# Performance work log

Hardware: AMD Instinct MI355X
Metric: run time of the kernel (lower is better)

The kernel has to match this reference:

```python
import jax, jax.numpy as jnp
import numpy as np

VOCAB = 100000
EMB = 128
EPS = 1e-12  # torch F.normalize eps

def setup_inputs() -> dict:
    key = jax.random.key(0)
    k1, k2, k3 = jax.random.split(key, 3)
    x = jax.random.randint(k1, (4096, 200), 0, VOCAB)
    W = jax.random.normal(k2, (EMB, VOCAB), dtype=jnp.float32) * 0.02
    b = jax.random.normal(k3, (EMB,), dtype=jnp.float32) * 0.02
    return {"x": x, "W": W, "b": b}

def reference(x, W, b):
    # one_hot(x) @ W.T + b  ==  W.T[x] + b  (row gather instead of dense matmul)
    table = W.T                      # [VOCAB, EMB]
    e = table[x] + b                 # [B, T, EMB]
    # L2 normalize along last dim (torch F.normalize p=2, eps=1e-12)
    n = jnp.sqrt(jnp.sum(e * e, axis=-1, keepdims=True))
    return e / jnp.maximum(n, EPS)
```

## Files before the change

### kernel.cpp

```cpp
#include <hip/hip_runtime.h>
#include <stdint.h>

#define EMB 128

typedef unsigned short ushort_t;
typedef ushort_t us8 __attribute__((ext_vector_type(8)));
typedef float f4 __attribute__((ext_vector_type(4)));

static __device__ __forceinline__ float bf2f(ushort_t h) {
    union { unsigned int u; float f; } cvt;
    cvt.u = ((unsigned int)h) << 16;
    return cvt.f;
}

static __device__ __forceinline__ ushort_t f2bf(float f) {
    union { float f; unsigned int u; } cvt;
    cvt.f = f;
    unsigned int u = cvt.u;
    unsigned int r = u + 0x7fffu + ((u >> 16) & 1u);
    return (ushort_t)(r >> 16);
}

__global__ __launch_bounds__(256) void build_table_f32_kernel(
    const float* __restrict__ W, const float* __restrict__ b,
    float* __restrict__ N, int vocab)
{
    __shared__ float tile[EMB][33];
    __shared__ float part[8][32];
    __shared__ float scale_s[32];

    const int v0 = blockIdx.x * 32;
    const int tx = threadIdx.x;
    const int ty = threadIdx.y;

    const int v  = v0 + tx;
    const bool vok = (v < vocab);

    #pragma unroll
    for (int e = ty; e < EMB; e += 8) {
        float w = vok ? W[(size_t)e * vocab + v] : 0.0f;
        tile[e][tx] = w + b[e];
    }
    __syncthreads();

    float ss = 0.0f;
    #pragma unroll
    for (int j = 0; j < 16; ++j) {
        float t = tile[ty * 16 + j][tx];
        ss += t * t;
    }
    part[ty][tx] = ss;
    __syncthreads();

    if (ty == 0) {
        float s = 0.0f;
        #pragma unroll
        for (int j = 0; j < 8; ++j) s += part[j][tx];
        scale_s[tx] = 1.0f / fmaxf(sqrtf(s), 1e-12f);
    }
    __syncthreads();

    const int tid = ty * 32 + tx;
    #pragma unroll
    for (int c = 0; c < 4; ++c) {
        const int chunk = tid + c * 256;
        const int r = chunk >> 5;
        const int q = chunk & 31;
        const int vv = v0 + r;
        if (vv < vocab) {
            const float sc = scale_s[r];
            f4 o;
            #pragma unroll
            for (int j = 0; j < 4; ++j) o[j] = tile[q * 4 + j][r] * sc;
            *(f4*)(N + (size_t)vv * EMB + q * 4) = o;
        }
    }
}

static __device__ __forceinline__ int detect_i64(const int* __restrict__ x32) {
    __shared__ int is64_s;
    if (threadIdx.x < 64) {
        int w = x32[2 * threadIdx.x + 1];
        unsigned long long nz = __ballot(w != 0);
        if (threadIdx.x == 0) is64_s = (nz == 0ULL) ? 1 : 0;
    }
    __syncthreads();
    return is64_s;
}

__global__ __launch_bounds__(256) void gather_copy_f32_kernel(
    const int* __restrict__ x, const float* __restrict__ N,
    float* __restrict__ out, int n_tokens, int vocab)
{
    const int is64 = detect_i64(x);
    const int tid   = blockIdx.x * blockDim.x + threadIdx.x;
    const int token = tid >> 4;
    const int l     = tid & 15;
    if (token >= n_tokens) return;

    int v = is64 ? x[2 * token] : x[token];
    v = min(max(v, 0), vocab - 1);

    const float* src = N + (size_t)v * EMB + l * 8;
    f4 a = *(const f4*)src;
    f4 c = *(const f4*)(src + 4);

    float* dst = out + (size_t)token * EMB + l * 8;
    __builtin_nontemporal_store(a, (f4*)dst);
    __builtin_nontemporal_store(c, (f4*)(dst + 4));
}

__global__ __launch_bounds__(256) void transpose_bf16_kernel(
    const float* __restrict__ W, ushort_t* __restrict__ Wt, int vocab)
{
    __shared__ float tile[32][33];
    const int v0 = blockIdx.x * 32;
    const int e0 = blockIdx.y * 32;
    const int tx = threadIdx.x;
    const int ty = threadIdx.y;

    #pragma unroll
    for (int i = 0; i < 32; i += 8) {
        int e = e0 + ty + i;
        int v = v0 + tx;
        if (e < EMB && v < vocab)
            tile[ty + i][tx] = W[(size_t)e * vocab + v];
    }
    __syncthreads();
    #pragma unroll
    for (int i = 0; i < 32; i += 8) {
        int v = v0 + ty + i;
        int e = e0 + tx;
        if (v < vocab && e < EMB)
            Wt[(size_t)v * EMB + e] = f2bf(tile[tx][ty + i]);
    }
}

static __device__ __forceinline__ void reduce_norm_store(
    float e[8], float* __restrict__ out, int token, int l)
{
    float ss = 0.0f;
    #pragma unroll
    for (int j = 0; j < 8; ++j) ss += e[j] * e[j];
    #pragma unroll
    for (int m = 1; m < 16; m <<= 1)
        ss += __shfl_xor(ss, m, 16);
    const float n = sqrtf(ss);
    const float scale = 1.0f / fmaxf(n, 1e-12f);

    f4 o0, o1;
    #pragma unroll
    for (int j = 0; j < 4; ++j) { o0[j] = e[j] * scale; o1[j] = e[j + 4] * scale; }
    float* dst = out + (size_t)token * EMB + l * 8;
    *(f4*)dst = o0;
    *(f4*)(dst + 4) = o1;
}

__global__ __launch_bounds__(256) void gather_norm_bf16_kernel(
    const int* __restrict__ x, const ushort_t* __restrict__ Wt,
    const float* __restrict__ b, float* __restrict__ out,
    int n_tokens, int vocab)
{
    const int is64 = detect_i64(x);
    const int tid   = blockIdx.x * blockDim.x + threadIdx.x;
    const int token = tid >> 4;
    const int l     = tid & 15;
    if (token >= n_tokens) return;

    int v = is64 ? x[2 * token] : x[token];
    v = min(max(v, 0), vocab - 1);

    us8 w  = *(const us8*)(Wt + (size_t)v * EMB + l * 8);
    f4 b0  = *(const f4*)(b + l * 8);
    f4 b1  = *(const f4*)(b + l * 8 + 4);

    float e[8];
    #pragma unroll
    for (int j = 0; j < 4; ++j) {
        e[j]     = bf2f(w[j])     + b0[j];
        e[j + 4] = bf2f(w[j + 4]) + b1[j];
    }
    reduce_norm_store(e, out, token, l);
}

__global__ __launch_bounds__(256) void gather_norm_direct_kernel(
    const int* __restrict__ x, const float* __restrict__ W,
    const float* __restrict__ b, float* __restrict__ out,
    int n_tokens, int vocab)
{
    const int is64 = detect_i64(x);
    const int tid   = blockIdx.x * blockDim.x + threadIdx.x;
    const int token = tid >> 4;
    const int l     = tid & 15;
    if (token >= n_tokens) return;

    int v = is64 ? x[2 * token] : x[token];
    v = min(max(v, 0), vocab - 1);

    f4 b0 = *(const f4*)(b + l * 8);
    f4 b1 = *(const f4*)(b + l * 8 + 4);

    float e[8];
    #pragma unroll
    for (int j = 0; j < 8; ++j) {
        float w = W[(size_t)(l * 8 + j) * vocab + v];
        float bj = (j < 4) ? b0[j & 3] : b1[j & 3];
        e[j] = w + bj;
    }
    reduce_norm_store(e, out, token, l);
}

extern "C" void kernel_launch(void* const* d_in, const int* in_sizes, int n_in,
                              void* d_out, int out_size, void* d_ws, size_t ws_size,
                              hipStream_t stream) {
    const int*   x = (const int*)d_in[0];
    const float* W = (const float*)d_in[1];
    const float* b = (const float*)d_in[2];
    float*     out = (float*)d_out;

    const int n_tokens = in_sizes[0];
    const int vocab    = in_sizes[1] / EMB;

    const size_t wt_f32_bytes  = (size_t)vocab * EMB * sizeof(float);
    const size_t wt_bf16_bytes = (size_t)vocab * EMB * sizeof(ushort_t);
    const int blocks = (n_tokens * 16 + 255) / 256;

    if (ws_size >= wt_f32_bytes) {
        float* N = (float*)d_ws;
        build_table_f32_kernel<<<dim3((vocab + 31) / 32), dim3(32, 8), 0, stream>>>(
            W, b, N, vocab);
        gather_copy_f32_kernel<<<blocks, 256, 0, stream>>>(x, N, out, n_tokens, vocab);
    } else if (ws_size >= wt_bf16_bytes) {
        ushort_t* Wt = (ushort_t*)d_ws;
        dim3 tb(32, 8);
        dim3 tg((vocab + 31) / 32, (EMB + 31) / 32);
        transpose_bf16_kernel<<<tg, tb, 0, stream>>>(W, Wt, vocab);
        gather_norm_bf16_kernel<<<blocks, 256, 0, stream>>>(x, Wt, b, out, n_tokens, vocab);
    } else {
        gather_norm_direct_kernel<<<blocks, 256, 0, stream>>>(x, W, b, out, n_tokens, vocab);
    }
}
```

Measured before the change: 540.2 us.

## Store normalized embedding table in fp16 and gather two tokens per thread

The precomputed bias-added, L2-normalized table is now stored in fp16 instead of fp32. This halves the table write traffic in the build kernel and the gather read traffic. The gather kernel also handles two tokens per thread (t0 and t0+half_n) to raise memory-level parallelism. The bf16 transpose fallback is removed, and the output is rounded to fp16 precision, which risks exceeding tolerance.

```diff
diff --git a/kernel.cpp b/kernel.cpp
--- a/kernel.cpp
+++ b/kernel.cpp
@@ -4,26 +4,13 @@
 #define EMB 128
 
 typedef unsigned short ushort_t;
-typedef ushort_t us8 __attribute__((ext_vector_type(8)));
+typedef _Float16 half_t;
+typedef half_t h8 __attribute__((ext_vector_type(8)));
 typedef float f4 __attribute__((ext_vector_type(4)));
 
-static __device__ __forceinline__ float bf2f(ushort_t h) {
-    union { unsigned int u; float f; } cvt;
-    cvt.u = ((unsigned int)h) << 16;
-    return cvt.f;
-}
-
-static __device__ __forceinline__ ushort_t f2bf(float f) {
-    union { float f; unsigned int u; } cvt;
-    cvt.f = f;
-    unsigned int u = cvt.u;
-    unsigned int r = u + 0x7fffu + ((u >> 16) & 1u);
-    return (ushort_t)(r >> 16);
-}
-
-__global__ __launch_bounds__(256) void build_table_f32_kernel(
+__global__ __launch_bounds__(256) void build_table_f16_kernel(
     const float* __restrict__ W, const float* __restrict__ b,
-    float* __restrict__ N, int vocab)
+    half_t* __restrict__ T, int vocab)
 {
     __shared__ float tile[EMB][33];
     __shared__ float part[8][32];
@@ -62,17 +49,18 @@
 
     const int tid = ty * 32 + tx;
     #pragma unroll
-    for (int c = 0; c < 4; ++c) {
+    for (int c = 0; c < 2; ++c) {
         const int chunk = tid + c * 256;
-        const int r = chunk >> 5;
-        const int q = chunk & 31;
+        const int r = chunk >> 4;
+        const int q = chunk & 15;
         const int vv = v0 + r;
         if (vv < vocab) {
             const float sc = scale_s[r];
-            f4 o;
+            h8 o;
             #pragma unroll
-            for (int j = 0; j < 4; ++j) o[j] = tile[q * 4 + j][r] * sc;
-            *(f4*)(N + (size_t)vv * EMB + q * 4) = o;
+            for (int j = 0; j < 8; ++j)
+                o[j] = (half_t)(tile[q * 8 + j][r] * sc);
+            *(h8*)(T + (size_t)vv * EMB + q * 8) = o;
         }
     }
 }
@@ -88,51 +76,43 @@
     return is64_s;
 }
 
-__global__ __launch_bounds__(256) void gather_copy_f32_kernel(
-    const int* __restrict__ x, const float* __restrict__ N,
+__global__ __launch_bounds__(256) void gather_copy_f16_kernel(
+    const int* __restrict__ x, const half_t* __restrict__ T,
     float* __restrict__ out, int n_tokens, int vocab)
 {
     const int is64 = detect_i64(x);
-    const int tid   = blockIdx.x * blockDim.x + threadIdx.x;
-    const int token = tid >> 4;
-    const int l     = tid & 15;
-    if (token >= n_tokens) return;
+    const int half_n = (n_tokens + 1) >> 1;
+    const int tid = blockIdx.x * blockDim.x + threadIdx.x;
+    const int t0  = tid >> 4;
+    const int l   = tid & 15;
+    if (t0 >= half_n) return;
 
-    int v = is64 ? x[2 * token] : x[token];
-    v = min(max(v, 0), vocab - 1);
+    const int t1  = t0 + half_n;
+    const int t1c = min(t1, n_tokens - 1);
 
-    const float* src = N + (size_t)v * EMB + l * 8;
-    f4 a = *(const f4*)src;
-    f4 c = *(const f4*)(src + 4);
+    int v0i = is64 ? x[2 * t0]  : x[t0];
+    int v1i = is64 ? x[2 * t1c] : x[t1c];
+    v0i = min(max(v0i, 0), vocab - 1);
+    v1i = min(max(v1i, 0), vocab - 1);
 
-    float* dst = out + (size_t)token * EMB + l * 8;
-    __builtin_nontemporal_store(a, (f4*)dst);
-    __builtin_nontemporal_store(c, (f4*)(dst + 4));
-}
+    const h8 w0 = *(const h8*)(T + (size_t)v0i * EMB + l * 8);
+    const h8 w1 = *(const h8*)(T + (size_t)v1i * EMB + l * 8);
 
-__global__ __launch_bounds__(256) void transpose_bf16_kernel(
-    const float* __restrict__ W, ushort_t* __restrict__ Wt, int vocab)
-{
-    __shared__ float tile[32][33];
-    const int v0 = blockIdx.x * 32;
-    const int e0 = blockIdx.y * 32;
-    const int tx = threadIdx.x;
-    const int ty = threadIdx.y;
+    f4 a0, c0, a1, c1;
+    #pragma unroll
+    for (int j = 0; j < 4; ++j) {
+        a0[j] = (float)w0[j];  c0[j] = (float)w0[j + 4];
+        a1[j] = (float)w1[j];  c1[j] = (float)w1[j + 4];
+    }
 
-    #pragma unroll
-    for (int i = 0; i < 32; i += 8) {
-        int e = e0 + ty + i;
-        int v = v0 + tx;
-        if (e < EMB && v < vocab)
-            tile[ty + i][tx] = W[(size_t)e * vocab + v];
-    }
-    __syncthreads();
-    #pragma unroll
-    for (int i = 0; i < 32; i += 8) {
-        int v = v0 + ty + i;
-        int e = e0 + tx;
-        if (v < vocab && e < EMB)
-            Wt[(size_t)v * EMB + e] = f2bf(tile[tx][ty + i]);
+    float* d0 = out + (size_t)t0 * EMB + l * 8;
+    __builtin_nontemporal_store(a0, (f4*)d0);
+    __builtin_nontemporal_store(c0, (f4*)(d0 + 4));
+
+    if (t1 < n_tokens) {
+        float* d1 = out + (size_t)t1 * EMB + l * 8;
+        __builtin_nontemporal_store(a1, (f4*)d1);
+        __builtin_nontemporal_store(c1, (f4*)(d1 + 4));
     }
 }
 
@@ -154,33 +134,6 @@
     float* dst = out + (size_t)token * EMB + l * 8;
     *(f4*)dst = o0;
     *(f4*)(dst + 4) = o1;
-}
-
-__global__ __launch_bounds__(256) void gather_norm_bf16_kernel(
-    const int* __restrict__ x, const ushort_t* __restrict__ Wt,
-    const float* __restrict__ b, float* __restrict__ out,
-    int n_tokens, int vocab)
-{
-    const int is64 = detect_i64(x);
-    const int tid   = blockIdx.x * blockDim.x + threadIdx.x;
-    const int token = tid >> 4;
-    const int l     = tid & 15;
-    if (token >= n_tokens) return;
-
-    int v = is64 ? x[2 * token] : x[token];
-    v = min(max(v, 0), vocab - 1);
-
-    us8 w  = *(const us8*)(Wt + (size_t)v * EMB + l * 8);
-    f4 b0  = *(const f4*)(b + l * 8);
-    f4 b1  = *(const f4*)(b + l * 8 + 4);
-
-    float e[8];
-    #pragma unroll
-    for (int j = 0; j < 4; ++j) {
-        e[j]     = bf2f(w[j])     + b0[j];
-        e[j + 4] = bf2f(w[j + 4]) + b1[j];
-    }
-    reduce_norm_store(e, out, token, l);
 }
 
 __global__ __launch_bounds__(256) void gather_norm_direct_kernel(
@@ -221,22 +174,17 @@
     const int n_tokens = in_sizes[0];
     const int vocab    = in_sizes[1] / EMB;
 
-    const size_t wt_f32_bytes  = (size_t)vocab * EMB * sizeof(float);
-    const size_t wt_bf16_bytes = (size_t)vocab * EMB * sizeof(ushort_t);
-    const int blocks = (n_tokens * 16 + 255) / 256;
+    const size_t t_f16_bytes = (size_t)vocab * EMB * sizeof(half_t);
 
-    if (ws_size >= wt_f32_bytes) {
-        float* N = (float*)d_ws;
-        build_table_f32_kernel<<<dim3((vocab + 31) / 32), dim3(32, 8), 0, stream>>>(
-            W, b, N, vocab);
-        gather_copy_f32_kernel<<<blocks, 256, 0, stream>>>(x, N, out, n_tokens, vocab);
-    } else if (ws_size >= wt_bf16_bytes) {
-        ushort_t* Wt = (ushort_t*)d_ws;
-        dim3 tb(32, 8);
-        dim3 tg((vocab + 31) / 32, (EMB + 31) / 32);
-        transpose_bf16_kernel<<<tg, tb, 0, stream>>>(W, Wt, vocab);
-        gather_norm_bf16_kernel<<<blocks, 256, 0, stream>>>(x, Wt, b, out, n_tokens, vocab);
+    if (ws_size >= t_f16_bytes) {
+        half_t* T = (half_t*)d_ws;
+        build_table_f16_kernel<<<dim3((vocab + 31) / 32), dim3(32, 8), 0, stream>>>(
+            W, b, T, vocab);
+        const int half_n = (n_tokens + 1) >> 1;
+        const int blocks = (half_n * 16 + 255) / 256;
+        gather_copy_f16_kernel<<<blocks, 256, 0, stream>>>(x, T, out, n_tokens, vocab);
     } else {
+        const int blocks = (n_tokens * 16 + 255) / 256;
         gather_norm_direct_kernel<<<blocks, 256, 0, stream>>>(x, W, b, out, n_tokens, vocab);
     }
 }
```

Measured after the change: 479.9 us. -11.2%, faster.
